# Optimization experiments

Hardware: AMD Instinct MI355X
Metric: run time of the kernel (lower is better)

## Reference

```python
import jax, jax.numpy as jnp
import numpy as np

B, E, F_IN = 8192, 64, 7
D, H = 64, 4           # feature_size, heads
HD = D // H            # features per head


def setup_inputs() -> dict:
    key = jax.random.key(0)
    ks = jax.random.split(key, 14)
    def lin(k, i, o):
        return jax.random.normal(k, (i, o), jnp.float32) * (1.0 / np.sqrt(i))
    return {
        "x": jax.random.normal(ks[0], (B, E, F_IN), jnp.float32),
        # ego embedding MLP (7->64->64, with bias)
        "ego_w0": lin(ks[1], F_IN, D), "ego_b0": jnp.zeros((D,), jnp.float32),
        "ego_w1": lin(ks[2], D, D),    "ego_b1": jnp.zeros((D,), jnp.float32),
        # others embedding MLP (separate weights)
        "oth_w0": lin(ks[3], F_IN, D), "oth_b0": jnp.zeros((D,), jnp.float32),
        "oth_w1": lin(ks[4], D, D),    "oth_b1": jnp.zeros((D,), jnp.float32),
        # attention projections (no bias)
        "Wk": lin(ks[5], D, D), "Wv": lin(ks[6], D, D),
        "Wq": lin(ks[7], D, D), "Wc": lin(ks[8], D, D),
    }


def _mlp(x, w0, b0, w1, b1):
    h = jax.nn.relu(x @ w0 + b0)
    return jax.nn.relu(h @ w1 + b1)


def reference(x, ego_w0, ego_b0, ego_w1, ego_b1,
              oth_w0, oth_b0, oth_w1, oth_b1, Wk, Wv, Wq, Wc):
    b = x.shape[0]
    mask = x[:, :, 0] < 0.5                       # [B, E] absent entities
    ego = _mlp(x[:, 0:1, :], ego_w0, ego_b0, ego_w1, ego_b1)   # [B, 1, D]
    others = _mlp(x[:, 1:, :], oth_w0, oth_b0, oth_w1, oth_b1)  # [B, E-1, D]
    input_all = jnp.concatenate([ego, others], axis=1)          # [B, E, D]

    # project and split heads -> [B, H, E, HD]
    k = (input_all @ Wk).reshape(b, E, H, HD).transpose(0, 2, 1, 3)
    v = (input_all @ Wv).reshape(b, E, H, HD).transpose(0, 2, 1, 3)
    q = (ego @ Wq).reshape(b, 1, H, HD).transpose(0, 2, 1, 3)   # [B, H, 1, HD]

    scores = jnp.einsum('bhqd,bhkd->bhqk', q, k) / np.sqrt(HD)  # [B, H, 1, E]
    scores = jnp.where(mask[:, None, None, :], -1e9, scores)
    p_attn = jax.nn.softmax(scores, axis=-1)
    out = jnp.einsum('bhqk,bhkd->bhqd', p_attn, v)              # [B, H, 1, HD]
    out = out.reshape(b, D)                                      # concat heads
    result = (out @ Wc + ego[:, 0, :]) * 0.5                     # [B, D]
    return result
```

## Files before the change

kernel.cpp:

```cpp
#include <hip/hip_runtime.h>
#include <hip/hip_bf16.h>


typedef __attribute__((ext_vector_type(8))) short short8;
typedef __attribute__((ext_vector_type(4))) short short4b;
typedef __attribute__((ext_vector_type(4))) float f32x4;

#define SY 72

#define WS_G    0
#define WS_EGW0 16384
#define WS_EGW1 16896
#define WS_WVT  20992
#define WS_WCT  25088
#define WS_W0T  29184
#define WS_W1T  29696

__device__ __forceinline__ short f2bs(float x) {
    __hip_bfloat16 h = __float2bfloat16(x);
    return __builtin_bit_cast(short, h);
}
__device__ __forceinline__ unsigned short f2u(float x) {
    __hip_bfloat16 h = __float2bfloat16(x);
    return __builtin_bit_cast(unsigned short, h);
}
__device__ __forceinline__ short8 ldws8(const unsigned short* p) {
    return *(const short8*)p;
}

__global__ void pack_ws(const float* __restrict__ ego_w0, const float* __restrict__ ego_w1,
                        const float* __restrict__ oth_w0, const float* __restrict__ oth_w1,
                        const float* __restrict__ Wk, const float* __restrict__ Wv,
                        const float* __restrict__ Wq, const float* __restrict__ Wc,
                        unsigned short* __restrict__ ws) {
    const int blk = blockIdx.x, t = threadIdx.x;
    if (blk < 256) {
        const int n = blk, h = n >> 6, f = n & 63, j = t;
        float a = 0.f;
#pragma unroll
        for (int d = 0; d < 16; ++d)
            a = fmaf(Wq[j * 64 + h * 16 + d], Wk[f * 64 + h * 16 + d], a);
        ws[WS_G + n * 64 + j] = f2u(a);
    } else {
        const int n = blk - 256, k = t;
        ws[WS_EGW1 + n * 64 + k] = f2u(ego_w1[k * 64 + n]);
        ws[WS_WVT  + n * 64 + k] = f2u(Wv[k * 64 + n]);
        ws[WS_WCT  + n * 64 + k] = f2u(Wc[k * 64 + n]);
        ws[WS_W1T  + n * 64 + k] = f2u(oth_w1[k * 64 + n]);
        if (k < 8) {
            ws[WS_EGW0 + n * 8 + k] = (k < 7) ? f2u(ego_w0[k * 64 + n]) : 0;
            ws[WS_W0T  + n * 8 + k] = (k < 7) ? f2u(oth_w0[k * 64 + n]) : 0;
        }
    }
}

__global__ __launch_bounds__(64, 2)
void ego_attn_kernel(const float* __restrict__ x,
                     const float* __restrict__ ego_b0, const float* __restrict__ ego_b1,
                     const float* __restrict__ oth_b0, const float* __restrict__ oth_b1,
                     const unsigned short* __restrict__ ws,
                     float* __restrict__ out)
{
    __shared__ __align__(16) short hy[64 * SY];
    __shared__ __align__(16) short chainbuf[4 * SY];
    __shared__ __align__(16) short kqb[16 * SY];
    __shared__ __align__(16) short pa[16 * SY];
    __shared__ __align__(16) short py[16 * SY];
    __shared__ __align__(16) short ob[4 * SY];
    __shared__ __align__(16) float mb[64];

    const int lane = threadIdx.x;
    const int lg = lane >> 4, ln = lane & 15;
    const int gb = blockIdx.x * 4;

    short8 w0f[4], w1f[2][4];
#pragma unroll
    for (int ct = 0; ct < 4; ++ct) {
        short8 z = {0, 0, 0, 0, 0, 0, 0, 0};
        w0f[ct] = (lg == 0) ? ldws8(ws + WS_W0T + (ct * 16 + ln) * 8) : z;
    }
#pragma unroll
    for (int kc = 0; kc < 2; ++kc)
#pragma unroll
        for (int ct = 0; ct < 4; ++ct)
            w1f[kc][ct] = ldws8(ws + WS_W1T + (ct * 16 + ln) * 64 + kc * 32 + lg * 8);
    float b0v[4], b1v[4], eb0v[4], eb1v[4];
#pragma unroll
    for (int ct = 0; ct < 4; ++ct) {
        b0v[ct]  = oth_b0[ct * 16 + ln];
        b1v[ct]  = oth_b1[ct * 16 + ln];
        eb0v[ct] = ego_b0[ct * 16 + ln];
        eb1v[ct] = ego_b1[ct * 16 + ln];
    }

    short8 xea = {0, 0, 0, 0, 0, 0, 0, 0};
    if (lg == 0 && ln < 4) {
        const float* xr = x + (size_t)(gb + ln) * 448;
#pragma unroll
        for (int i = 0; i < 7; ++i) xea[i] = f2bs(xr[i]);
    }
#pragma unroll
    for (int ct = 0; ct < 4; ++ct) {
        short8 z = {0, 0, 0, 0, 0, 0, 0, 0};
        const short8 bfr = (lg == 0) ? ldws8(ws + WS_EGW0 + (ct * 16 + ln) * 8) : z;
        f32x4 c = {eb0v[ct], eb0v[ct], eb0v[ct], eb0v[ct]};
        c = __builtin_amdgcn_mfma_f32_16x16x32_bf16(xea, bfr, c, 0, 0, 0);
        if (lg == 0) {
#pragma unroll
            for (int r = 0; r < 4; ++r)
                chainbuf[r * SY + ct * 16 + ln] = f2bs(fmaxf(c[r], 0.f));
        }
    }
    __syncthreads();
    short8 ha[2];
#pragma unroll
    for (int kc = 0; kc < 2; ++kc)
        ha[kc] = *(const short8*)&chainbuf[(ln & 3) * SY + kc * 32 + lg * 8];
    __syncthreads();

    float egoR[4][4];
#pragma unroll
    for (int ct = 0; ct < 4; ++ct) {
        f32x4 c = {eb1v[ct], eb1v[ct], eb1v[ct], eb1v[ct]};
#pragma unroll
        for (int kc = 0; kc < 2; ++kc) {
            const short8 bfr = ldws8(ws + WS_EGW1 + (ct * 16 + ln) * 64 + kc * 32 + lg * 8);
            c = __builtin_amdgcn_mfma_f32_16x16x32_bf16(ha[kc], bfr, c, 0, 0, 0);
        }
#pragma unroll
        for (int r = 0; r < 4; ++r) egoR[ct][r] = fmaxf(c[r], 0.f);
    }
    if (lg == 0) {
#pragma unroll
        for (int ct = 0; ct < 4; ++ct)
#pragma unroll
            for (int r = 0; r < 4; ++r)
                chainbuf[r * SY + ct * 16 + ln] = f2bs(egoR[ct][r]);
    }
    __syncthreads();
    short8 ea[2];
#pragma unroll
    for (int kc = 0; kc < 2; ++kc)
        ea[kc] = *(const short8*)&chainbuf[(ln & 3) * SY + kc * 32 + lg * 8];

#pragma unroll
    for (int ctg = 0; ctg < 16; ++ctg) {
        f32x4 c = {0.f, 0.f, 0.f, 0.f};
#pragma unroll
        for (int kc = 0; kc < 2; ++kc) {
            const short8 bfr = ldws8(ws + WS_G + (ctg * 16 + ln) * 64 + kc * 32 + lg * 8);
            c = __builtin_amdgcn_mfma_f32_16x16x32_bf16(ea[kc], bfr, c, 0, 0, 0);
        }
        if (lg == 0) {
            const int h = ctg >> 2, fc = (ctg & 3) * 16 + ln;
#pragma unroll
            for (int r = 0; r < 4; ++r)
                kqb[(r * 4 + h) * SY + fc] = f2bs(c[r] * 0.25f);
        }
    }
    __syncthreads();

#pragma unroll
    for (int i = 0; i < 4; ++i) {
        const float* xb = x + (size_t)(gb + i) * 448;
        mb[lane] = xb[lane * 7];

        short8 xa[4];
#pragma unroll
        for (int mt = 0; mt < 4; ++mt) {
            short8 v = {0, 0, 0, 0, 0, 0, 0, 0};
            if (lg == 0) {
                const float* xr = xb + (mt * 16 + ln) * 7;
#pragma unroll
                for (int k = 0; k < 7; ++k) v[k] = f2bs(xr[k]);
            }
            xa[mt] = v;
        }
#pragma unroll
        for (int mt = 0; mt < 4; ++mt)
#pragma unroll
            for (int ct = 0; ct < 4; ++ct) {
                f32x4 c = {b0v[ct], b0v[ct], b0v[ct], b0v[ct]};
                c = __builtin_amdgcn_mfma_f32_16x16x32_bf16(xa[mt], w0f[ct], c, 0, 0, 0);
#pragma unroll
                for (int r = 0; r < 4; ++r)
                    hy[(mt * 16 + lg * 4 + r) * SY + ct * 16 + ln] = f2bs(fmaxf(c[r], 0.f));
            }
        __syncthreads();
        short8 a2[4][2];
#pragma unroll
        for (int mt = 0; mt < 4; ++mt)
#pragma unroll
            for (int kc = 0; kc < 2; ++kc)
                a2[mt][kc] = *(const short8*)&hy[(mt * 16 + ln) * SY + kc * 32 + lg * 8];
        __syncthreads();
#pragma unroll
        for (int ct = 0; ct < 4; ++ct)
#pragma unroll
            for (int mt = 0; mt < 4; ++mt) {
                f32x4 c = {b1v[ct], b1v[ct], b1v[ct], b1v[ct]};
                c = __builtin_amdgcn_mfma_f32_16x16x32_bf16(a2[mt][0], w1f[0][ct], c, 0, 0, 0);
                c = __builtin_amdgcn_mfma_f32_16x16x32_bf16(a2[mt][1], w1f[1][ct], c, 0, 0, 0);
#pragma unroll
                for (int r = 0; r < 4; ++r)
                    hy[(mt * 16 + lg * 4 + r) * SY + ct * 16 + ln] = f2bs(fmaxf(c[r], 0.f));
            }
        if (lg == 0) {
#pragma unroll
            for (int ct = 0; ct < 4; ++ct)
                hy[ct * 16 + ln] = f2bs(egoR[ct][i]);
        }
        __syncthreads();
        short8 ya[4][2];
#pragma unroll
        for (int mt = 0; mt < 4; ++mt)
#pragma unroll
            for (int kc = 0; kc < 2; ++kc)
                ya[mt][kc] = *(const short8*)&hy[(mt * 16 + ln) * SY + kc * 32 + lg * 8];
        short8 kb[2];
#pragma unroll
        for (int kc = 0; kc < 2; ++kc)
            kb[kc] = *(const short8*)&kqb[(i * 4 + (ln & 3)) * SY + kc * 32 + lg * 8];

        float sv[16];
        float m = -3e38f;
#pragma unroll
        for (int mt = 0; mt < 4; ++mt) {
            f32x4 c = {0.f, 0.f, 0.f, 0.f};
            c = __builtin_amdgcn_mfma_f32_16x16x32_bf16(ya[mt][0], kb[0], c, 0, 0, 0);
            c = __builtin_amdgcn_mfma_f32_16x16x32_bf16(ya[mt][1], kb[1], c, 0, 0, 0);
            const float4 mk = *(const float4*)&mb[mt * 16 + lg * 4];
            const float mkv[4] = {mk.x, mk.y, mk.z, mk.w};
#pragma unroll
            for (int r = 0; r < 4; ++r) {
                float s = c[r];
                if (mkv[r] < 0.5f) s = -1e9f;
                sv[mt * 4 + r] = s;
                m = fmaxf(m, s);
            }
        }
        m = fmaxf(m, __shfl_xor(m, 16));
        m = fmaxf(m, __shfl_xor(m, 32));
        float sum = 0.f;
#pragma unroll
        for (int k = 0; k < 16; ++k) { sv[k] = __expf(sv[k] - m); sum += sv[k]; }
        sum += __shfl_xor(sum, 16);
        sum += __shfl_xor(sum, 32);
        const float inv = 1.f / sum;
#pragma unroll
        for (int mt = 0; mt < 4; ++mt) {
            short4b pk;
#pragma unroll
            for (int r = 0; r < 4; ++r) pk[r] = f2bs(sv[mt * 4 + r] * inv);
            *(short4b*)&pa[ln * SY + mt * 16 + lg * 4] = pk;
        }
        __syncthreads();
        short8 pf[2];
#pragma unroll
        for (int kc = 0; kc < 2; ++kc)
            pf[kc] = *(const short8*)&pa[ln * SY + kc * 32 + lg * 8];
#pragma unroll
        for (int ct = 0; ct < 4; ++ct) {
            f32x4 c = {0.f, 0.f, 0.f, 0.f};
#pragma unroll
            for (int kc = 0; kc < 2; ++kc) {
                short8 yv;
#pragma unroll
                for (int j = 0; j < 8; ++j)
                    yv[j] = hy[(kc * 32 + lg * 8 + j) * SY + ct * 16 + ln];
                c = __builtin_amdgcn_mfma_f32_16x16x32_bf16(pf[kc], yv, c, 0, 0, 0);
            }
            if (lg == 0) {
#pragma unroll
                for (int r = 0; r < 4; ++r)
                    py[(r * 4 + i) * SY + ct * 16 + ln] = f2bs(c[r]);
            }
        }
        __syncthreads();
    }

#pragma unroll
    for (int ct = 0; ct < 4; ++ct) {
        short8 af[2];
#pragma unroll
        for (int kc = 0; kc < 2; ++kc)
            af[kc] = *(const short8*)&py[(ct * 4 + (ln & 3)) * SY + kc * 32 + lg * 8];
        f32x4 c = {0.f, 0.f, 0.f, 0.f};
#pragma unroll
        for (int kc = 0; kc < 2; ++kc) {
            const short8 bfr = ldws8(ws + WS_WVT + (ct * 16 + ln) * 64 + kc * 32 + lg * 8);
            c = __builtin_amdgcn_mfma_f32_16x16x32_bf16(af[kc], bfr, c, 0, 0, 0);
        }
        if (lg == 0) {
#pragma unroll
            for (int r = 0; r < 4; ++r)
                ob[r * SY + ct * 16 + ln] = f2bs(c[r]);
        }
    }
    __syncthreads();
    short8 oa[2];
#pragma unroll
    for (int kc = 0; kc < 2; ++kc)
        oa[kc] = *(const short8*)&ob[(ln & 3) * SY + kc * 32 + lg * 8];
#pragma unroll
    for (int ct = 0; ct < 4; ++ct) {
        f32x4 c = {0.f, 0.f, 0.f, 0.f};
#pragma unroll
        for (int kc = 0; kc < 2; ++kc) {
            const short8 bfr = ldws8(ws + WS_WCT + (ct * 16 + ln) * 64 + kc * 32 + lg * 8);
            c = __builtin_amdgcn_mfma_f32_16x16x32_bf16(oa[kc], bfr, c, 0, 0, 0);
        }
        if (lg == 0) {
#pragma unroll
            for (int r = 0; r < 4; ++r)
                out[(size_t)(gb + r) * 64 + ct * 16 + ln] = (c[r] + egoR[ct][r]) * 0.5f;
        }
    }
}

extern "C" void kernel_launch(void* const* d_in, const int* in_sizes, int n_in,
                              void* d_out, int out_size, void* d_ws, size_t ws_size,
                              hipStream_t stream) {
    const float* x      = (const float*)d_in[0];
    const float* ego_w0 = (const float*)d_in[1];
    const float* ego_b0 = (const float*)d_in[2];
    const float* ego_w1 = (const float*)d_in[3];
    const float* ego_b1 = (const float*)d_in[4];
    const float* oth_w0 = (const float*)d_in[5];
    const float* oth_b0 = (const float*)d_in[6];
    const float* oth_w1 = (const float*)d_in[7];
    const float* oth_b1 = (const float*)d_in[8];
    const float* Wk     = (const float*)d_in[9];
    const float* Wv     = (const float*)d_in[10];
    const float* Wq     = (const float*)d_in[11];
    const float* Wc     = (const float*)d_in[12];

    unsigned short* ws = (unsigned short*)d_ws;
    pack_ws<<<320, 64, 0, stream>>>(ego_w0, ego_w1, oth_w0, oth_w1,
                                    Wk, Wv, Wq, Wc, ws);
    ego_attn_kernel<<<2048, 64, 0, stream>>>(
        x, ego_b0, ego_b1, oth_b0, oth_b1, ws, (float*)d_out);
}
```

Baseline: 121.2 us.

## Split per-block work across four wavefronts by output column tile

```diff
diff --git a/kernel.cpp b/kernel.cpp
--- a/kernel.cpp
+++ b/kernel.cpp
@@ -54,7 +54,7 @@
     }
 }
 
-__global__ __launch_bounds__(64, 2)
+__global__ __launch_bounds__(256, 6)
 void ego_attn_kernel(const float* __restrict__ x,
                      const float* __restrict__ ego_b0, const float* __restrict__ ego_b1,
                      const float* __restrict__ oth_b0, const float* __restrict__ oth_b1,
@@ -67,48 +67,45 @@
     __shared__ __align__(16) short pa[16 * SY];
     __shared__ __align__(16) short py[16 * SY];
     __shared__ __align__(16) short ob[4 * SY];
-    __shared__ __align__(16) float mb[64];
-
-    const int lane = threadIdx.x;
+    __shared__ __align__(16) float mbuf[4][64];
+
+    const int tid  = threadIdx.x;
+    const int w    = tid >> 6;
+    const int lane = tid & 63;
     const int lg = lane >> 4, ln = lane & 15;
     const int gb = blockIdx.x * 4;
 
-    short8 w0f[4], w1f[2][4];
-#pragma unroll
-    for (int ct = 0; ct < 4; ++ct) {
-        short8 z = {0, 0, 0, 0, 0, 0, 0, 0};
-        w0f[ct] = (lg == 0) ? ldws8(ws + WS_W0T + (ct * 16 + ln) * 8) : z;
-    }
+    const short8 z8 = {0, 0, 0, 0, 0, 0, 0, 0};
+
+    short8 w0f[4];
+#pragma unroll
+    for (int ct = 0; ct < 4; ++ct)
+        w0f[ct] = (lg == 0) ? ldws8(ws + WS_W0T + (ct * 16 + ln) * 8) : z8;
+    short8 w1w[2];
 #pragma unroll
     for (int kc = 0; kc < 2; ++kc)
-#pragma unroll
-        for (int ct = 0; ct < 4; ++ct)
-            w1f[kc][ct] = ldws8(ws + WS_W1T + (ct * 16 + ln) * 64 + kc * 32 + lg * 8);
-    float b0v[4], b1v[4], eb0v[4], eb1v[4];
-#pragma unroll
-    for (int ct = 0; ct < 4; ++ct) {
-        b0v[ct]  = oth_b0[ct * 16 + ln];
-        b1v[ct]  = oth_b1[ct * 16 + ln];
-        eb0v[ct] = ego_b0[ct * 16 + ln];
-        eb1v[ct] = ego_b1[ct * 16 + ln];
-    }
-
-    short8 xea = {0, 0, 0, 0, 0, 0, 0, 0};
+        w1w[kc] = ldws8(ws + WS_W1T + (w * 16 + ln) * 64 + kc * 32 + lg * 8);
+    float b0v[4];
+#pragma unroll
+    for (int ct = 0; ct < 4; ++ct) b0v[ct] = oth_b0[ct * 16 + ln];
+    const float b1w  = oth_b1[w * 16 + ln];
+    const float eb0w = ego_b0[w * 16 + ln];
+    const float eb1w = ego_b1[w * 16 + ln];
+
+    short8 xea = z8;
     if (lg == 0 && ln < 4) {
         const float* xr = x + (size_t)(gb + ln) * 448;
 #pragma unroll
-        for (int i = 0; i < 7; ++i) xea[i] = f2bs(xr[i]);
-    }
-#pragma unroll
-    for (int ct = 0; ct < 4; ++ct) {
-        short8 z = {0, 0, 0, 0, 0, 0, 0, 0};
-        const short8 bfr = (lg == 0) ? ldws8(ws + WS_EGW0 + (ct * 16 + ln) * 8) : z;
-        f32x4 c = {eb0v[ct], eb0v[ct], eb0v[ct], eb0v[ct]};
+        for (int k = 0; k < 7; ++k) xea[k] = f2bs(xr[k]);
+    }
+    {
+        const short8 bfr = (lg == 0) ? ldws8(ws + WS_EGW0 + (w * 16 + ln) * 8) : z8;
+        f32x4 c = {eb0w, eb0w, eb0w, eb0w};
         c = __builtin_amdgcn_mfma_f32_16x16x32_bf16(xea, bfr, c, 0, 0, 0);
         if (lg == 0) {
 #pragma unroll
             for (int r = 0; r < 4; ++r)
-                chainbuf[r * SY + ct * 16 + ln] = f2bs(fmaxf(c[r], 0.f));
+                chainbuf[r * SY + w * 16 + ln] = f2bs(fmaxf(c[r], 0.f));
         }
     }
     __syncthreads();
@@ -118,24 +115,21 @@
         ha[kc] = *(const short8*)&chainbuf[(ln & 3) * SY + kc * 32 + lg * 8];
     __syncthreads();
 
-    float egoR[4][4];
-#pragma unroll
-    for (int ct = 0; ct < 4; ++ct) {
-        f32x4 c = {eb1v[ct], eb1v[ct], eb1v[ct], eb1v[ct]};
+    float egoR[4];
+    {
+        f32x4 c = {eb1w, eb1w, eb1w, eb1w};
 #pragma unroll
         for (int kc = 0; kc < 2; ++kc) {
-            const short8 bfr = ldws8(ws + WS_EGW1 + (ct * 16 + ln) * 64 + kc * 32 + lg * 8);
+            const short8 bfr = ldws8(ws + WS_EGW1 + (w * 16 + ln) * 64 + kc * 32 + lg * 8);
             c = __builtin_amdgcn_mfma_f32_16x16x32_bf16(ha[kc], bfr, c, 0, 0, 0);
         }
 #pragma unroll
-        for (int r = 0; r < 4; ++r) egoR[ct][r] = fmaxf(c[r], 0.f);
-    }
-    if (lg == 0) {
-#pragma unroll
-        for (int ct = 0; ct < 4; ++ct)
-#pragma unroll
-            for (int r = 0; r < 4; ++r)
-                chainbuf[r * SY + ct * 16 + ln] = f2bs(egoR[ct][r]);
+        for (int r = 0; r < 4; ++r) egoR[r] = fmaxf(c[r], 0.f);
+        if (lg == 0) {
+#pragma unroll
+            for (int r = 0; r < 4; ++r)
+                chainbuf[r * SY + w * 16 + ln] = f2bs(egoR[r]);
+        }
     }
     __syncthreads();
     short8 ea[2];
@@ -144,49 +138,42 @@
         ea[kc] = *(const short8*)&chainbuf[(ln & 3) * SY + kc * 32 + lg * 8];
 
 #pragma unroll
-    for (int ctg = 0; ctg < 16; ++ctg) {
+    for (int q = 0; q < 4; ++q) {
         f32x4 c = {0.f, 0.f, 0.f, 0.f};
 #pragma unroll
         for (int kc = 0; kc < 2; ++kc) {
-            const short8 bfr = ldws8(ws + WS_G + (ctg * 16 + ln) * 64 + kc * 32 + lg * 8);
+            const short8 bfr = ldws8(ws + WS_G + (w * 64 + q * 16 + ln) * 64 + kc * 32 + lg * 8);
             c = __builtin_amdgcn_mfma_f32_16x16x32_bf16(ea[kc], bfr, c, 0, 0, 0);
         }
         if (lg == 0) {
-            const int h = ctg >> 2, fc = (ctg & 3) * 16 + ln;
-#pragma unroll
-            for (int r = 0; r < 4; ++r)
-                kqb[(r * 4 + h) * SY + fc] = f2bs(c[r] * 0.25f);
-        }
-    }
+#pragma unroll
+            for (int r = 0; r < 4; ++r)
+                kqb[(r * 4 + w) * SY + q * 16 + ln] = f2bs(c[r] * 0.25f);
+        }
+    }
+    mbuf[w][lane] = x[(size_t)(gb + w) * 448 + lane * 7];
     __syncthreads();
 
 #pragma unroll
     for (int i = 0; i < 4; ++i) {
         const float* xb = x + (size_t)(gb + i) * 448;
-        mb[lane] = xb[lane * 7];
-
-        short8 xa[4];
-#pragma unroll
-        for (int mt = 0; mt < 4; ++mt) {
-            short8 v = {0, 0, 0, 0, 0, 0, 0, 0};
-            if (lg == 0) {
-                const float* xr = xb + (mt * 16 + ln) * 7;
-#pragma unroll
-                for (int k = 0; k < 7; ++k) v[k] = f2bs(xr[k]);
-            }
-            xa[mt] = v;
-        }
-#pragma unroll
-        for (int mt = 0; mt < 4; ++mt)
-#pragma unroll
-            for (int ct = 0; ct < 4; ++ct) {
-                f32x4 c = {b0v[ct], b0v[ct], b0v[ct], b0v[ct]};
-                c = __builtin_amdgcn_mfma_f32_16x16x32_bf16(xa[mt], w0f[ct], c, 0, 0, 0);
-#pragma unroll
-                for (int r = 0; r < 4; ++r)
-                    hy[(mt * 16 + lg * 4 + r) * SY + ct * 16 + ln] = f2bs(fmaxf(c[r], 0.f));
-            }
-        __syncthreads();
+
+        short8 xaw = z8;
+        if (lg == 0) {
+            const float* xr = xb + (w * 16 + ln) * 7;
+#pragma unroll
+            for (int k = 0; k < 7; ++k) xaw[k] = f2bs(xr[k]);
+        }
+#pragma unroll
+        for (int ct = 0; ct < 4; ++ct) {
+            f32x4 c = {b0v[ct], b0v[ct], b0v[ct], b0v[ct]};
+            c = __builtin_amdgcn_mfma_f32_16x16x32_bf16(xaw, w0f[ct], c, 0, 0, 0);
+#pragma unroll
+            for (int r = 0; r < 4; ++r)
+                hy[(w * 16 + lg * 4 + r) * SY + ct * 16 + ln] = f2bs(fmaxf(c[r], 0.f));
+        }
+        __syncthreads();
+
         short8 a2[4][2];
 #pragma unroll
         for (int mt = 0; mt < 4; ++mt)
@@ -195,125 +182,116 @@
                 a2[mt][kc] = *(const short8*)&hy[(mt * 16 + ln) * SY + kc * 32 + lg * 8];
         __syncthreads();
 #pragma unroll
-        for (int ct = 0; ct < 4; ++ct)
+        for (int mt = 0; mt < 4; ++mt) {
+            f32x4 c = {b1w, b1w, b1w, b1w};
+            c = __builtin_amdgcn_mfma_f32_16x16x32_bf16(a2[mt][0], w1w[0], c, 0, 0, 0);
+            c = __builtin_amdgcn_mfma_f32_16x16x32_bf16(a2[mt][1], w1w[1], c, 0, 0, 0);
+#pragma unroll
+            for (int r = 0; r < 4; ++r)
+                hy[(mt * 16 + lg * 4 + r) * SY + w * 16 + ln] = f2bs(fmaxf(c[r], 0.f));
+        }
+        if (lg == 0)
+            hy[w * 16 + ln] = f2bs(egoR[i]);
+        __syncthreads();
+
+        if (w == i) {
+            short8 kb[2];
+#pragma unroll
+            for (int kc = 0; kc < 2; ++kc)
+                kb[kc] = *(const short8*)&kqb[(i * 4 + (ln & 3)) * SY + kc * 32 + lg * 8];
+            float sv[16];
+            float m = -3e38f;
 #pragma unroll
             for (int mt = 0; mt < 4; ++mt) {
-                f32x4 c = {b1v[ct], b1v[ct], b1v[ct], b1v[ct]};
-                c = __builtin_amdgcn_mfma_f32_16x16x32_bf16(a2[mt][0], w1f[0][ct], c, 0, 0, 0);
-                c = __builtin_amdgcn_mfma_f32_16x16x32_bf16(a2[mt][1], w1f[1][ct], c, 0, 0, 0);
-#pragma unroll
-                for (int r = 0; r < 4; ++r)
-                    hy[(mt * 16 + lg * 4 + r) * SY + ct * 16 + ln] = f2bs(fmaxf(c[r], 0.f));
+                f32x4 c = {0.f, 0.f, 0.f, 0.f};
+                const short8 ya0 = *(const short8*)&hy[(mt * 16 + ln) * SY + 0 * 32 + lg * 8];
+                const short8 ya1 = *(const short8*)&hy[(mt * 16 + ln) * SY + 1 * 32 + lg * 8];
+                c = __builtin_amdgcn_mfma_f32_16x16x32_bf16(ya0, kb[0], c, 0, 0, 0);
+                c = __builtin_amdgcn_mfma_f32_16x16x32_bf16(ya1, kb[1], c, 0, 0, 0);
+                const float4 mk = *(const float4*)&mbuf[i][mt * 16 + lg * 4];
+                const float mkv[4] = {mk.x, mk.y, mk.z, mk.w};
+#pragma unroll
+                for (int r = 0; r < 4; ++r) {
+                    float s = c[r];
+                    if (mkv[r] < 0.5f) s = -1e9f;
+                    sv[mt * 4 + r] = s;
+                    m = fmaxf(m, s);
+                }
             }
-        if (lg == 0) {
-#pragma unroll
-            for (int ct = 0; ct < 4; ++ct)
-                hy[ct * 16 + ln] = f2bs(egoR[ct][i]);
-        }
-        __syncthreads();
-        short8 ya[4][2];
-#pragma unroll
-        for (int mt = 0; mt < 4; ++mt)
-#pragma unroll
-            for (int kc = 0; kc < 2; ++kc)
-                ya[mt][kc] = *(const short8*)&hy[(mt * 16 + ln) * SY + kc * 32 + lg * 8];
-        short8 kb[2];
-#pragma unroll
-        for (int kc = 0; kc < 2; ++kc)
-            kb[kc] = *(const short8*)&kqb[(i * 4 + (ln & 3)) * SY + kc * 32 + lg * 8];
-
-        float sv[16];
-        float m = -3e38f;
-#pragma unroll
-        for (int mt = 0; mt < 4; ++mt) {
-            f32x4 c = {0.f, 0.f, 0.f, 0.f};
-            c = __builtin_amdgcn_mfma_f32_16x16x32_bf16(ya[mt][0], kb[0], c, 0, 0, 0);
-            c = __builtin_amdgcn_mfma_f32_16x16x32_bf16(ya[mt][1], kb[1], c, 0, 0, 0);
-            const float4 mk = *(const float4*)&mb[mt * 16 + lg * 4];
-            const float mkv[4] = {mk.x, mk.y, mk.z, mk.w};
-#pragma unroll
-            for (int r = 0; r < 4; ++r) {
-                float s = c[r];
-                if (mkv[r] < 0.5f) s = -1e9f;
-                sv[mt * 4 + r] = s;
-                m = fmaxf(m, s);
+            m = fmaxf(m, __shfl_xor(m, 16));
+            m = fmaxf(m, __shfl_xor(m, 32));
+            float sum = 0.f;
+#pragma unroll
+            for (int k = 0; k < 16; ++k) { sv[k] = __expf(sv[k] - m); sum += sv[k]; }
+            sum += __shfl_xor(sum, 16);
+            sum += __shfl_xor(sum, 32);
+            const float inv = 1.f / sum;
+#pragma unroll
+            for (int mt = 0; mt < 4; ++mt) {
+                short4b pk;
+#pragma unroll
+                for (int r = 0; r < 4; ++r) pk[r] = f2bs(sv[mt * 4 + r] * inv);
+                *(short4b*)&pa[ln * SY + mt * 16 + lg * 4] = pk;
             }
         }
-        m = fmaxf(m, __shfl_xor(m, 16));
-        m = fmaxf(m, __shfl_xor(m, 32));
-        float sum = 0.f;
-#pragma unroll
-        for (int k = 0; k < 16; ++k) { sv[k] = __expf(sv[k] - m); sum += sv[k]; }
-        sum += __shfl_xor(sum, 16);
-        sum += __shfl_xor(sum, 32);
-        const float inv = 1.f / sum;
-#pragma unroll
-        for (int mt = 0; mt < 4; ++mt) {
-            short4b pk;
-#pragma unroll
-            for (int r = 0; r < 4; ++r) pk[r] = f2bs(sv[mt * 4 + r] * inv);
-            *(short4b*)&pa[ln * SY + mt * 16 + lg * 4] = pk;
-        }
-        __syncthreads();
+        __syncthreads();
+
         short8 pf[2];
 #pragma unroll
         for (int kc = 0; kc < 2; ++kc)
             pf[kc] = *(const short8*)&pa[ln * SY + kc * 32 + lg * 8];
-#pragma unroll
-        for (int ct = 0; ct < 4; ++ct) {
+        {
             f32x4 c = {0.f, 0.f, 0.f, 0.f};
 #pragma unroll
             for (int kc = 0; kc < 2; ++kc) {
                 short8 yv;
 #pragma unroll
                 for (int j = 0; j < 8; ++j)
-                    yv[j] = hy[(kc * 32 + lg * 8 + j) * SY + ct * 16 + ln];
+                    yv[j] = hy[(kc * 32 + lg * 8 + j) * SY + w * 16 + ln];
                 c = __builtin_amdgcn_mfma_f32_16x16x32_bf16(pf[kc], yv, c, 0, 0, 0);
             }
             if (lg == 0) {
 #pragma unroll
                 for (int r = 0; r < 4; ++r)
-                    py[(r * 4 + i) * SY + ct * 16 + ln] = f2bs(c[r]);
+                    py[(r * 4 + i) * SY + w * 16 + ln] = f2bs(c[r]);
             }
         }
         __syncthreads();
     }
 
-#pragma unroll
-    for (int ct = 0; ct < 4; ++ct) {
+    {
         short8 af[2];
 #pragma unroll
         for (int kc = 0; kc < 2; ++kc)
-            af[kc] = *(const short8*)&py[(ct * 4 + (ln & 3)) * SY + kc * 32 + lg * 8];
+            af[kc] = *(const short8*)&py[(w * 4 + (ln & 3)) * SY + kc * 32 + lg * 8];
         f32x4 c = {0.f, 0.f, 0.f, 0.f};
 #pragma unroll
         for (int kc = 0; kc < 2; ++kc) {
-            const short8 bfr = ldws8(ws + WS_WVT + (ct * 16 + ln) * 64 + kc * 32 + lg * 8);
+            const short8 bfr = ldws8(ws + WS_WVT + (w * 16 + ln) * 64 + kc * 32 + lg * 8);
             c = __builtin_amdgcn_mfma_f32_16x16x32_bf16(af[kc], bfr, c, 0, 0, 0);
         }
         if (lg == 0) {
 #pragma unroll
             for (int r = 0; r < 4; ++r)
-                ob[r * SY + ct * 16 + ln] = f2bs(c[r]);
-        }
-    }
-    __syncthreads();
-    short8 oa[2];
-#pragma unroll
-    for (int kc = 0; kc < 2; ++kc)
-        oa[kc] = *(const short8*)&ob[(ln & 3) * SY + kc * 32 + lg * 8];
-#pragma unroll
-    for (int ct = 0; ct < 4; ++ct) {
+                ob[r * SY + w * 16 + ln] = f2bs(c[r]);
+        }
+    }
+    __syncthreads();
+    {
+        short8 oa[2];
+#pragma unroll
+        for (int kc = 0; kc < 2; ++kc)
+            oa[kc] = *(const short8*)&ob[(ln & 3) * SY + kc * 32 + lg * 8];
         f32x4 c = {0.f, 0.f, 0.f, 0.f};
 #pragma unroll
         for (int kc = 0; kc < 2; ++kc) {
-            const short8 bfr = ldws8(ws + WS_WCT + (ct * 16 + ln) * 64 + kc * 32 + lg * 8);
+            const short8 bfr = ldws8(ws + WS_WCT + (w * 16 + ln) * 64 + kc * 32 + lg * 8);
             c = __builtin_amdgcn_mfma_f32_16x16x32_bf16(oa[kc], bfr, c, 0, 0, 0);
         }
         if (lg == 0) {
 #pragma unroll
             for (int r = 0; r < 4; ++r)
-                out[(size_t)(gb + r) * 64 + ct * 16 + ln] = (c[r] + egoR[ct][r]) * 0.5f;
+                out[(size_t)(gb + r) * 64 + w * 16 + ln] = (c[r] + egoR[r]) * 0.5f;
         }
     }
 }
@@ -338,6 +316,6 @@
     unsigned short* ws = (unsigned short*)d_ws;
     pack_ws<<<320, 64, 0, stream>>>(ego_w0, ego_w1, oth_w0, oth_w1,
                                     Wk, Wv, Wq, Wc, ws);
-    ego_attn_kernel<<<2048, 64, 0, stream>>>(
+    ego_attn_kernel<<<2048, 256, 0, stream>>>(
         x, ego_b0, ego_b1, oth_b0, oth_b1, ws, (float*)d_out);
 }
```

Result: slower. 148.2 us (+22.2%).
